# Performance work log

Hardware: AMD Instinct MI355X
Metric: run time of the kernel (lower is better)

The kernel has to match this reference:

```python
import jax, jax.numpy as jnp
import numpy as np


def setup_inputs() -> dict:
    key = jax.random.key(0)
    k1, k2 = jax.random.split(key)
    B, T, D, K = 16, 4096, 1024, 512
    h = jax.random.normal(k1, (B, T, D), dtype=jnp.float32)
    codebook = jax.random.normal(k2, (K, D), dtype=jnp.float32)
    return {"h": h, "codebook": codebook}


def reference(h, codebook):
    """SAMMCodebook.encode: nearest-codeword indices via squared L2 distance.

    h: [B, T, D]; codebook: [K, D] -> z: [B, T] int32
    """
    B, T, D = h.shape
    h_flat = h.reshape(-1, D)                                  # [N, D]
    h_sq = jnp.sum(h_flat * h_flat, axis=-1, keepdims=True)    # [N, 1]
    c_sq = jnp.sum(codebook * codebook, axis=-1)[None, :]      # [1, K]
    # dist[n,k] = ||h_n||^2 + ||c_k||^2 - 2 <h_n, c_k>
    dist = h_sq + c_sq - 2.0 * (h_flat @ codebook.T)           # [N, K]
    z = jnp.argmin(dist, axis=-1).reshape(B, T)
    return z.astype(jnp.int32)
```

## Files before the change

kernel.cpp:

```cpp
#include <hip/hip_runtime.h>


#define D_DIM 1024
#define K_CB  512
#define DELTA 4.0f
#define MAXC_IN 15
#define FULLSCAN 0xFFFFu

typedef __attribute__((ext_vector_type(8))) short short8;
typedef __attribute__((ext_vector_type(4))) float floatx4;

#define WS_CBB  0ull
#define WS_CSQ  1048576ull

typedef const unsigned int __attribute__((address_space(1)))* gaddr_t;
typedef unsigned int __attribute__((address_space(3)))* laddr_t;
static __device__ __forceinline__ void async_copy16(const void* g, void* l) {
    __builtin_amdgcn_global_load_lds((gaddr_t)g, (laddr_t)l, 16, 0, 0);
}

static __device__ __forceinline__ unsigned f2bf(float f) {
    unsigned u = __builtin_bit_cast(unsigned, f);
    return (u + 0x7FFFu + ((u >> 16) & 1u)) >> 16;
}

__global__ __launch_bounds__(256)
void prep_kernel(const float* __restrict__ cb, unsigned short* __restrict__ cbb,
                 float* __restrict__ csq) {
    __shared__ float red[4];
    const int k = blockIdx.x, t = threadIdx.x;
    const float4 v = *(const float4*)(cb + (size_t)k * D_DIM + t * 4);
    uint2 u;
    u.x = f2bf(v.x) | (f2bf(v.y) << 16);
    u.y = f2bf(v.z) | (f2bf(v.w) << 16);
    *(uint2*)(cbb + (size_t)k * D_DIM + t * 4) = u;
    float s = v.x * v.x + v.y * v.y + v.z * v.z + v.w * v.w;
    #pragma unroll
    for (int off = 32; off > 0; off >>= 1) s += __shfl_down(s, off, 64);
    if ((t & 63) == 0) red[t >> 6] = s;
    __syncthreads();
    if (t == 0) csq[k] = red[0] + red[1] + red[2] + red[3];
}

__global__ __launch_bounds__(256, 2)
void coarse_kernel(const float* __restrict__ h,
                   const unsigned short* __restrict__ cbb,
                   const float* __restrict__ csq,
                   const float* __restrict__ cb,
                   int* __restrict__ out) {
    __shared__ unsigned char smem[73728] __attribute__((aligned(16)));
    unsigned short* As = (unsigned short*)smem;
    unsigned short* Bs = (unsigned short*)(smem + 8192);

    const int tid = threadIdx.x;
    const int w = tid >> 6, lane = tid & 63;
    const int l15 = lane & 15, kq = lane >> 4;
    const size_t row0 = (size_t)blockIdx.x * 64;
    const int wc_ = w * 128;

    const int qp8 = (kq ^ ((l15 >> 1) & 3)) * 8;

    const int ar = tid >> 2, aql = tid & 3;
    const float* gA = h + (row0 + ar) * D_DIM + aql * 8;
    const int awoff = ar * 32 + (aql ^ ((ar >> 1) & 3)) * 8;

    const int qsrc = (lane & 3) ^ ((lane >> 3) & 3);
    const int brow = w * 128 + (lane >> 2);
    const unsigned char* cbb_b = (const unsigned char*)cbb;
    const size_t bsrc_base = ((size_t)brow * D_DIM + qsrc * 8) * 2;

    floatx4 acc[4][8];
    #pragma unroll
    for (int i = 0; i < 4; ++i)
        #pragma unroll
        for (int j = 0; j < 8; ++j) acc[i][j] = (floatx4){0.f, 0.f, 0.f, 0.f};

    float4 va0, va1;

#define ISSUE_B(dkn, par) \
    _Pragma("unroll") \
    for (int j = 0; j < 8; ++j) \
        async_copy16(cbb_b + bsrc_base + (size_t)j * (16 * D_DIM * 2) + (size_t)(dkn) * 2, \
                     Bs + (par) * 16384 + (w * 128 + j * 16) * 32);

#define LOAD_A(dkn) do { \
    va0 = *(const float4*)(gA + (dkn)); \
    va1 = *(const float4*)(gA + (dkn) + 4); \
} while (0)

#define PUB_A(par) do { \
    uint4 u; \
    u.x = f2bf(va0.x) | (f2bf(va0.y) << 16); \
    u.y = f2bf(va0.z) | (f2bf(va0.w) << 16); \
    u.z = f2bf(va1.x) | (f2bf(va1.y) << 16); \
    u.w = f2bf(va1.z) | (f2bf(va1.w) << 16); \
    *(uint4*)(As + (par) * 2048 + awoff) = u; \
} while (0)

    LOAD_A(0);
    ISSUE_B(0, 0);
    asm volatile("s_waitcnt vmcnt(8)" ::: "memory");
    __builtin_amdgcn_sched_barrier(0);
    PUB_A(0);
    asm volatile("s_waitcnt lgkmcnt(0)" ::: "memory");
    __builtin_amdgcn_s_barrier();
    __builtin_amdgcn_sched_barrier(0);

#define STEP(p, s, LAST) do { \
    if (!(LAST)) { \
        LOAD_A(((s) + 1) * 32); \
        ISSUE_B(((s) + 1) * 32, (p) ^ 1); \
        asm volatile("s_waitcnt vmcnt(10)" ::: "memory");   \
    } else { \
        asm volatile("s_waitcnt vmcnt(0)" ::: "memory"); \
    } \
    __builtin_amdgcn_sched_barrier(0); \
    short8 a[4], b[8]; \
    _Pragma("unroll") \
    for (int rt = 0; rt < 4; ++rt) \
        a[rt] = *(const short8*)(As + (p) * 2048 + (rt * 16 + l15) * 32 + qp8); \
    _Pragma("unroll") \
    for (int ct = 0; ct < 8; ++ct) \
        b[ct] = *(const short8*)(Bs + (p) * 16384 + (wc_ + ct * 16 + l15) * 32 + qp8); \
    __builtin_amdgcn_s_setprio(1); \
    _Pragma("unroll") \
    for (int rt = 0; rt < 4; ++rt) \
        _Pragma("unroll") \
        for (int ct = 0; ct < 8; ++ct) \
            acc[rt][ct] = __builtin_amdgcn_mfma_f32_16x16x32_bf16( \
                a[rt], b[ct], acc[rt][ct], 0, 0, 0); \
    __builtin_amdgcn_s_setprio(0); \
    if (!(LAST)) { \
        asm volatile("s_waitcnt vmcnt(8)" ::: "memory");    \
        __builtin_amdgcn_sched_barrier(0); \
        PUB_A((p) ^ 1); \
    } \
    asm volatile("s_waitcnt lgkmcnt(0)" ::: "memory");      \
    __builtin_amdgcn_s_barrier(); \
    __builtin_amdgcn_sched_barrier(0); \
} while (0)

    for (int s2 = 0; s2 < 15; ++s2) {
        STEP(0, 2 * s2, false);
        STEP(1, 2 * s2 + 1, false);
    }
    STEP(0, 30, false);
    STEP(1, 31, true);

#undef STEP
#undef PUB_A
#undef LOAD_A
#undef ISSUE_B

    float k1[16], k2[16];
    unsigned cpk[16];
    #pragma unroll
    for (int i = 0; i < 16; ++i) { k1[i] = 3.4e38f; k2[i] = 3.4e38f; cpk[i] = 0; }
    #pragma unroll
    for (int ct = 0; ct < 8; ++ct) {
        const int col = wc_ + ct * 16 + l15;
        const float cq = csq[col];
        #pragma unroll
        for (int rt = 0; rt < 4; ++rt)
            #pragma unroll
            for (int reg = 0; reg < 4; ++reg) {
                const float s = fmaf(-2.0f, acc[rt][ct][reg], cq);
                const int ri = rt * 4 + reg;
                if (s < k1[ri]) {
                    k2[ri] = k1[ri]; k1[ri] = s;
                    cpk[ri] = (cpk[ri] << 16) | (unsigned)col;
                } else if (s < k2[ri]) {
                    k2[ri] = s;
                    cpk[ri] = (cpk[ri] & 0xFFFFu) | ((unsigned)col << 16);
                }
            }
    }

    float* mval = (float*)smem;
    int*   mcol = (int*)(smem + 33024);
    unsigned short* ccnt  = (unsigned short*)(smem + 66048);
    unsigned short* clist = (unsigned short*)(smem + 66176);
    __syncthreads();
    #pragma unroll
    for (int rt = 0; rt < 4; ++rt)
        #pragma unroll
        for (int reg = 0; reg < 4; ++reg) {
            const int ri = rt * 4 + reg;
            const int r = rt * 16 + kq * 4 + reg;
            const int e = (w * 16 + l15) * 2;
            mval[r * 129 + e] = k1[ri];
            mcol[r * 129 + e] = (int)(cpk[ri] & 0xFFFFu);
            mval[r * 129 + e + 1] = k2[ri];
            mcol[r * 129 + e + 1] = (int)(cpk[ri] >> 16);
        }
    __syncthreads();

    if (tid < 64) {
        const int r = tid;
        float bv = mval[r * 129]; int bc = mcol[r * 129];
        for (int e = 1; e < 128; ++e) {
            const float v = mval[r * 129 + e];
            const int   c = mcol[r * 129 + e];
            if (v < bv || (v == bv && c < bc)) { bv = v; bc = c; }
        }
        const float thr = bv + DELTA;
        int others = 0;
        for (int e = 0; e < 128; ++e) {
            const float v = mval[r * 129 + e];
            const int   c = mcol[r * 129 + e];
            if (v < thr && c != bc) {
                if (others < MAXC_IN) clist[r * 16 + 1 + others] = (unsigned short)c;
                ++others;
            }
        }
        if (others == 0) {
            out[row0 + r] = bc;
            ccnt[r] = 0;
        } else if (others <= MAXC_IN) {
            clist[r * 16] = (unsigned short)bc;
            ccnt[r] = (unsigned short)(others + 1);
        } else {
            ccnt[r] = (unsigned short)FULLSCAN;
        }
    }
    __syncthreads();

    for (int r = w; r < 64; r += 4) {
        const unsigned cnt = ccnt[r];
        if (cnt == 0) continue;
        const size_t grow = row0 + r;
        const float* hrow = h + grow * D_DIM;
        float4 hv[4];
        #pragma unroll
        for (int j = 0; j < 4; ++j)
            hv[j] = *(const float4*)(hrow + j * 256 + lane * 4);
        float bs = 3.4e38f; int bc = 0x7fffffff;
        const bool full = (cnt == FULLSCAN);
        const int total = full ? K_CB : (int)cnt;
        for (int i = 0; i < total; ++i) {
            const int c = full ? i : (int)clist[r * 16 + i];
            const float* crow = cb + (size_t)c * D_DIM;
            float d = 0.0f;
            #pragma unroll
            for (int j = 0; j < 4; ++j) {
                const float4 cv = *(const float4*)(crow + j * 256 + lane * 4);
                d = fmaf(hv[j].x, cv.x, d);
                d = fmaf(hv[j].y, cv.y, d);
                d = fmaf(hv[j].z, cv.z, d);
                d = fmaf(hv[j].w, cv.w, d);
            }
            #pragma unroll
            for (int off = 32; off > 0; off >>= 1) d += __shfl_down(d, off, 64);
            d = __shfl(d, 0, 64);
            const float sc = fmaf(-2.0f, d, csq[c]);
            if (sc < bs || (sc == bs && c < bc)) { bs = sc; bc = c; }
        }
        if (lane == 0) out[grow] = bc;
    }
}

extern "C" void kernel_launch(void* const* d_in, const int* in_sizes, int n_in,
                              void* d_out, int out_size, void* d_ws, size_t ws_size,
                              hipStream_t stream) {
    const float* h  = (const float*)d_in[0];
    const float* cb = (const float*)d_in[1];
    int* out = (int*)d_out;
    unsigned char* ws = (unsigned char*)d_ws;
    const int nrows = in_sizes[0] / D_DIM;

    unsigned short* cbb = (unsigned short*)(ws + WS_CBB);
    float* csq = (float*)(ws + WS_CSQ);

    prep_kernel<<<dim3(K_CB), dim3(256), 0, stream>>>(cb, cbb, csq);
    coarse_kernel<<<dim3(nrows / 64), dim3(256), 0, stream>>>(
        h, cbb, csq, cb, out);
}
```

Before: 463.0 us.

## Use 512-thread blocks covering 128 rows to share codebook tiles

Blocks grow from 256 to 512 threads and from 64 to 128 rows. Eight waves are split into two row halves by four column slices, so each codebook bf16 tile in LDS serves twice as many rows and per-wave B loads are halved. The hand-tuned vmcnt waits and sched barriers are replaced with plain __syncthreads, which gives up the fine-grained overlap of global loads with MFMA. The candidate reduction now runs in two serial halves, and occupancy drops to one block per CU.

```diff
diff --git a/kernel.cpp b/kernel.cpp
--- a/kernel.cpp
+++ b/kernel.cpp
@@ -42,21 +42,23 @@
     if (t == 0) csq[k] = red[0] + red[1] + red[2] + red[3];
 }
 
-__global__ __launch_bounds__(256, 2)
+__global__ __launch_bounds__(512, 1)
 void coarse_kernel(const float* __restrict__ h,
                    const unsigned short* __restrict__ cbb,
                    const float* __restrict__ csq,
                    const float* __restrict__ cb,
                    int* __restrict__ out) {
-    __shared__ unsigned char smem[73728] __attribute__((aligned(16)));
+    __shared__ unsigned char smem[81920] __attribute__((aligned(16)));
     unsigned short* As = (unsigned short*)smem;
-    unsigned short* Bs = (unsigned short*)(smem + 8192);
+    unsigned short* Bs = (unsigned short*)(smem + 16384);
 
     const int tid = threadIdx.x;
     const int w = tid >> 6, lane = tid & 63;
     const int l15 = lane & 15, kq = lane >> 4;
-    const size_t row0 = (size_t)blockIdx.x * 64;
-    const int wc_ = w * 128;
+    const int cs = w & 3, rh = w >> 2;
+    const size_t row0 = (size_t)blockIdx.x * 128;
+    const int wc_ = cs * 128;
+    const int rbase = rh * 64;
 
     const int qp8 = (kq ^ ((l15 >> 1) & 3)) * 8;
 
@@ -65,7 +67,7 @@
     const int awoff = ar * 32 + (aql ^ ((ar >> 1) & 3)) * 8;
 
     const int qsrc = (lane & 3) ^ ((lane >> 3) & 3);
-    const int brow = w * 128 + (lane >> 2);
+    const int brow = cs * 128 + rh * 64 + (lane >> 2);
     const unsigned char* cbb_b = (const unsigned char*)cbb;
     const size_t bsrc_base = ((size_t)brow * D_DIM + qsrc * 8) * 2;
 
@@ -79,14 +81,9 @@
 
 #define ISSUE_B(dkn, par) \
     _Pragma("unroll") \
-    for (int j = 0; j < 8; ++j) \
+    for (int j = 0; j < 4; ++j) \
         async_copy16(cbb_b + bsrc_base + (size_t)j * (16 * D_DIM * 2) + (size_t)(dkn) * 2, \
-                     Bs + (par) * 16384 + (w * 128 + j * 16) * 32);
-
-#define LOAD_A(dkn) do { \
-    va0 = *(const float4*)(gA + (dkn)); \
-    va1 = *(const float4*)(gA + (dkn) + 4); \
-} while (0)
+                     Bs + (par) * 16384 + (cs * 128 + rh * 64 + j * 16) * 32);
 
 #define PUB_A(par) do { \
     uint4 u; \
@@ -94,31 +91,19 @@
     u.y = f2bf(va0.z) | (f2bf(va0.w) << 16); \
     u.z = f2bf(va1.x) | (f2bf(va1.y) << 16); \
     u.w = f2bf(va1.z) | (f2bf(va1.w) << 16); \
-    *(uint4*)(As + (par) * 2048 + awoff) = u; \
+    *(uint4*)(As + (par) * 4096 + awoff) = u; \
 } while (0)
-
-    LOAD_A(0);
-    ISSUE_B(0, 0);
-    asm volatile("s_waitcnt vmcnt(8)" ::: "memory");
-    __builtin_amdgcn_sched_barrier(0);
-    PUB_A(0);
-    asm volatile("s_waitcnt lgkmcnt(0)" ::: "memory");
-    __builtin_amdgcn_s_barrier();
-    __builtin_amdgcn_sched_barrier(0);
 
 #define STEP(p, s, LAST) do { \
     if (!(LAST)) { \
-        LOAD_A(((s) + 1) * 32); \
+        va0 = *(const float4*)(gA + ((s) + 1) * 32); \
+        va1 = *(const float4*)(gA + ((s) + 1) * 32 + 4); \
         ISSUE_B(((s) + 1) * 32, (p) ^ 1); \
-        asm volatile("s_waitcnt vmcnt(10)" ::: "memory");   \
-    } else { \
-        asm volatile("s_waitcnt vmcnt(0)" ::: "memory"); \
     } \
-    __builtin_amdgcn_sched_barrier(0); \
     short8 a[4], b[8]; \
     _Pragma("unroll") \
     for (int rt = 0; rt < 4; ++rt) \
-        a[rt] = *(const short8*)(As + (p) * 2048 + (rt * 16 + l15) * 32 + qp8); \
+        a[rt] = *(const short8*)(As + (p) * 4096 + (rbase + rt * 16 + l15) * 32 + qp8); \
     _Pragma("unroll") \
     for (int ct = 0; ct < 8; ++ct) \
         b[ct] = *(const short8*)(Bs + (p) * 16384 + (wc_ + ct * 16 + l15) * 32 + qp8); \
@@ -130,26 +115,23 @@
             acc[rt][ct] = __builtin_amdgcn_mfma_f32_16x16x32_bf16( \
                 a[rt], b[ct], acc[rt][ct], 0, 0, 0); \
     __builtin_amdgcn_s_setprio(0); \
-    if (!(LAST)) { \
-        asm volatile("s_waitcnt vmcnt(8)" ::: "memory");    \
-        __builtin_amdgcn_sched_barrier(0); \
-        PUB_A((p) ^ 1); \
-    } \
-    asm volatile("s_waitcnt lgkmcnt(0)" ::: "memory");      \
-    __builtin_amdgcn_s_barrier(); \
-    __builtin_amdgcn_sched_barrier(0); \
+    if (!(LAST)) PUB_A((p) ^ 1); \
+    __syncthreads(); \
 } while (0)
 
-    for (int s2 = 0; s2 < 15; ++s2) {
+    va0 = *(const float4*)(gA);
+    va1 = *(const float4*)(gA + 4);
+    ISSUE_B(0, 0);
+    PUB_A(0);
+    __syncthreads();
+
+    for (int s2 = 0; s2 < 16; ++s2) {
         STEP(0, 2 * s2, false);
-        STEP(1, 2 * s2 + 1, false);
-    }
-    STEP(0, 30, false);
-    STEP(1, 31, true);
+        STEP(1, 2 * s2 + 1, (s2 == 15));
+    }
 
 #undef STEP
 #undef PUB_A
-#undef LOAD_A
 #undef ISSUE_B
 
     float k1[16], k2[16];
@@ -179,53 +161,58 @@
     float* mval = (float*)smem;
     int*   mcol = (int*)(smem + 33024);
     unsigned short* ccnt  = (unsigned short*)(smem + 66048);
-    unsigned short* clist = (unsigned short*)(smem + 66176);
+    unsigned short* clist = (unsigned short*)(smem + 66304);
+
+    for (int H = 0; H < 2; ++H) {
+        __syncthreads();
+        if (rh == H) {
+            #pragma unroll
+            for (int rt = 0; rt < 4; ++rt)
+                #pragma unroll
+                for (int reg = 0; reg < 4; ++reg) {
+                    const int ri = rt * 4 + reg;
+                    const int r = rt * 16 + kq * 4 + reg;
+                    const int e = (cs * 16 + l15) * 2;
+                    mval[r * 129 + e] = k1[ri];
+                    mcol[r * 129 + e] = (int)(cpk[ri] & 0xFFFFu);
+                    mval[r * 129 + e + 1] = k2[ri];
+                    mcol[r * 129 + e + 1] = (int)(cpk[ri] >> 16);
+                }
+        }
+        __syncthreads();
+        if (tid < 64) {
+            const int r = tid;
+            const int gr = H * 64 + r;
+            float bv = mval[r * 129]; int bc = mcol[r * 129];
+            for (int e = 1; e < 128; ++e) {
+                const float v = mval[r * 129 + e];
+                const int   c = mcol[r * 129 + e];
+                if (v < bv || (v == bv && c < bc)) { bv = v; bc = c; }
+            }
+            const float thr = bv + DELTA;
+            int others = 0;
+            for (int e = 0; e < 128; ++e) {
+                const float v = mval[r * 129 + e];
+                const int   c = mcol[r * 129 + e];
+                if (v < thr && c != bc) {
+                    if (others < MAXC_IN) clist[gr * 16 + 1 + others] = (unsigned short)c;
+                    ++others;
+                }
+            }
+            if (others == 0) {
+                out[row0 + gr] = bc;
+                ccnt[gr] = 0;
+            } else if (others <= MAXC_IN) {
+                clist[gr * 16] = (unsigned short)bc;
+                ccnt[gr] = (unsigned short)(others + 1);
+            } else {
+                ccnt[gr] = (unsigned short)FULLSCAN;
+            }
+        }
+    }
     __syncthreads();
-    #pragma unroll
-    for (int rt = 0; rt < 4; ++rt)
-        #pragma unroll
-        for (int reg = 0; reg < 4; ++reg) {
-            const int ri = rt * 4 + reg;
-            const int r = rt * 16 + kq * 4 + reg;
-            const int e = (w * 16 + l15) * 2;
-            mval[r * 129 + e] = k1[ri];
-            mcol[r * 129 + e] = (int)(cpk[ri] & 0xFFFFu);
-            mval[r * 129 + e + 1] = k2[ri];
-            mcol[r * 129 + e + 1] = (int)(cpk[ri] >> 16);
-        }
-    __syncthreads();
-
-    if (tid < 64) {
-        const int r = tid;
-        float bv = mval[r * 129]; int bc = mcol[r * 129];
-        for (int e = 1; e < 128; ++e) {
-            const float v = mval[r * 129 + e];
-            const int   c = mcol[r * 129 + e];
-            if (v < bv || (v == bv && c < bc)) { bv = v; bc = c; }
-        }
-        const float thr = bv + DELTA;
-        int others = 0;
-        for (int e = 0; e < 128; ++e) {
-            const float v = mval[r * 129 + e];
-            const int   c = mcol[r * 129 + e];
-            if (v < thr && c != bc) {
-                if (others < MAXC_IN) clist[r * 16 + 1 + others] = (unsigned short)c;
-                ++others;
-            }
-        }
-        if (others == 0) {
-            out[row0 + r] = bc;
-            ccnt[r] = 0;
-        } else if (others <= MAXC_IN) {
-            clist[r * 16] = (unsigned short)bc;
-            ccnt[r] = (unsigned short)(others + 1);
-        } else {
-            ccnt[r] = (unsigned short)FULLSCAN;
-        }
-    }
-    __syncthreads();
-
-    for (int r = w; r < 64; r += 4) {
+
+    for (int r = w; r < 128; r += 8) {
         const unsigned cnt = ccnt[r];
         if (cnt == 0) continue;
         const size_t grow = row0 + r;
@@ -272,6 +259,6 @@
     float* csq = (float*)(ws + WS_CSQ);
 
     prep_kernel<<<dim3(K_CB), dim3(256), 0, stream>>>(cb, cbb, csq);
-    coarse_kernel<<<dim3(nrows / 64), dim3(256), 0, stream>>>(
+    coarse_kernel<<<dim3(nrows / 128), dim3(512), 0, stream>>>(
         h, cbb, csq, cb, out);
 }
```

Result: slower. 484.2 us (+4.6%).
